# Optimization experiments

Measured on AMD Instinct MI355X. Metric: run time of the kernel, lower is better.

The kernel has to match this reference:

```python
import jax, jax.numpy as jnp
import numpy as np

B, NORB, N_UP, N_DN, HIDDEN = 1024, 128, 32, 32, 4096


def setup_inputs() -> dict:
    rng = np.random.default_rng(0)
    # Build valid occupancy configs: exactly N_UP up-electrons (bit 0) and
    # N_DN down-electrons (bit 1) per sample. Encoding: 0=empty,1=up,2=dn,3=updn.
    up_order = np.argsort(rng.random((B, NORB)), axis=1)
    dn_order = np.argsort(rng.random((B, NORB)), axis=1)
    up_bit = np.zeros((B, NORB), np.int32)
    dn_bit = np.zeros((B, NORB), np.int32)
    np.put_along_axis(up_bit, up_order[:, :N_UP], 1, axis=1)
    np.put_along_axis(dn_bit, dn_order[:, :N_DN], 1, axis=1)
    x = jnp.asarray(up_bit + 2 * dn_bit, dtype=jnp.int32)

    key = jax.random.key(0)
    k1, k2, k3 = jax.random.split(key, 3)
    orbitals = jax.random.normal(k1, (NORB, N_UP), jnp.float32)
    W1 = jax.random.normal(k2, (4 * NORB, HIDDEN), jnp.float32) / np.sqrt(4 * NORB)
    b1 = jnp.zeros((HIDDEN,), jnp.float32)
    W2 = jax.random.normal(k3, (HIDDEN, NORB * N_UP), jnp.float32) / np.sqrt(HIDDEN)
    b2 = jnp.zeros((NORB * N_UP,), jnp.float32)
    return {"x": x, "orbitals": orbitals, "W1": W1, "b1": b1, "W2": W2, "b2": b2}


def _occupancies_to_electrons(x, n_up, n_dn):
    # Per-spin sorted positions of occupied orbitals. Stable argsort on the
    # inverted mask keeps occupied sites first, in ascending orbital order.
    up_mask = (x & 1) == 1
    dn_mask = (x & 2) == 2
    y_up = jnp.argsort(jnp.where(up_mask, 0, 1), axis=-1, stable=True)[:, :n_up]
    y_dn = jnp.argsort(jnp.where(dn_mask, 0, 1), axis=-1, stable=True)[:, :n_dn]
    return y_up, y_dn


def reference(x, orbitals, W1, b1, W2, b2):
    Bsz, norb = x.shape
    n_up = orbitals.shape[1]

    # correction_fun: MLP on one-hot config -> [B, norb, n_up]
    h = jax.nn.one_hot(x, 4, dtype=W1.dtype).reshape(Bsz, -1)  # [B, 4*norb]
    h = jax.nn.relu(h @ W1 + b1)                               # [B, hidden]
    corrections = (h @ W2 + b2).reshape(Bsz, norb, n_up)       # [B, norb, n_up]

    y_up, y_dn = _occupancies_to_electrons(x, n_up, n_up)
    y_up = y_up[..., None]  # [B, n_up, 1]
    y_dn = y_dn[..., None]

    # gather orbital rows + correction rows per electron (spin-symmetric orbitals)
    phi_up = jnp.take_along_axis(orbitals[None], y_up, axis=1)  # [B, n_up, n_up]
    phi_dn = jnp.take_along_axis(orbitals[None], y_dn, axis=1)
    d_up = jnp.take_along_axis(corrections, y_up, axis=1)
    d_dn = jnp.take_along_axis(corrections, y_dn, axis=1)

    s_up, log_det_up = jnp.linalg.slogdet(phi_up + d_up)
    s_dn, log_det_dn = jnp.linalg.slogdet(phi_dn + d_dn)
    return log_det_up + log_det_dn + jnp.log(s_up * s_dn + 0j)  # complex [B]
```

## Files before the change

kernel.cpp:

```cpp
#include <hip/hip_runtime.h>
#include <cmath>

#define B_SZ  1024
#define NORB  128
#define NUP   32
#define HID   4096
#define NCORR (NORB * NUP)
#define K1    (4 * NORB)

typedef short  bf16x8 __attribute__((ext_vector_type(8)));
typedef float  f32x4  __attribute__((ext_vector_type(4)));

__device__ __forceinline__ unsigned short f2bf_rne(float f) {
    unsigned int u = __float_as_uint(f);
    u += 0x7FFFu + ((u >> 16) & 1u);
    return (unsigned short)(u >> 16);
}

__global__ __launch_bounds__(256) void k_splitW(const float* __restrict__ W,
                                                unsigned short* __restrict__ Bph,
                                                unsigned short* __restrict__ Bpl,
                                                int ktTot) {
    __shared__ float tile[64][33];
    int n0 = blockIdx.x * 32, k0 = blockIdx.y * 64;
    int t = threadIdx.x;

    int rl = t >> 3, c4 = (t & 7) * 4;
#pragma unroll
    for (int i = 0; i < 2; ++i) {
        int kl = rl + 32 * i;
        float4 v = *(const float4*)(W + (size_t)(k0 + kl) * 4096 + n0 + c4);
        tile[kl][c4 + 0] = v.x; tile[kl][c4 + 1] = v.y;
        tile[kl][c4 + 2] = v.z; tile[kl][c4 + 3] = v.w;
    }
    __syncthreads();

    int nl = t & 31, kg = t >> 5;
    int nt = (n0 + nl) >> 4;
    int kt = (k0 >> 5) + (kg >> 2);
    int lane_o = (kg & 3) * 16 + (nl & 15);
    size_t o = (((size_t)nt * ktTot + kt) * 64 + lane_o) * 8;

    unsigned short hi8[8], lo8[8];
#pragma unroll
    for (int j = 0; j < 8; ++j) {
        float v = tile[kg * 8 + j][nl];
        unsigned short hi = f2bf_rne(v);
        float fhi = __uint_as_float((unsigned int)hi << 16);
        hi8[j] = hi;
        lo8[j] = f2bf_rne(v - fhi);
    }
    *(bf16x8*)(Bph + o) = *(bf16x8*)hi8;
    *(bf16x8*)(Bpl + o) = *(bf16x8*)lo8;
}

__global__ __launch_bounds__(256, 2) void k_hidden3(const int* __restrict__ x,
                                                    const unsigned short* __restrict__ Bph,
                                                    const unsigned short* __restrict__ Bpl,
                                                    const float* __restrict__ b1,
                                                    unsigned short* __restrict__ h_hi,
                                                    unsigned short* __restrict__ h_lo) {
    __shared__ unsigned int sxp[64][8];
    __shared__ unsigned short BF[2][4][4][512];
    __shared__ float Ht[64][132];

    int n0 = blockIdx.x * 128;
    int m0 = blockIdx.y * 64;
    int t = threadIdx.x;
    int w = t >> 6, lane = t & 63;
    int lm = lane & 15, kq = lane >> 4;
    int wn = w * 32;

#pragma unroll
    for (int i = 0; i < 2; ++i) {
        int id = t + 256 * i;
        int row = id >> 3, d = id & 7;
        const int* src = x + (size_t)(m0 + row) * NORB + d * 16;
        unsigned int dw = 0;
#pragma unroll
        for (int b = 0; b < 16; ++b) dw |= ((unsigned int)(src[b] & 3)) << (2 * b);
        sxp[row][d] = dw;
    }

    int nt0 = (n0 + wn) >> 4;
    const unsigned short* bh0 = Bph + (size_t)nt0 * (16 * 512) + (size_t)lane * 8;
    const unsigned short* bh1 = Bph + (size_t)(nt0 + 1) * (16 * 512) + (size_t)lane * 8;
    const unsigned short* bl0 = Bpl + (size_t)nt0 * (16 * 512) + (size_t)lane * 8;
    const unsigned short* bl1 = Bpl + (size_t)(nt0 + 1) * (16 * 512) + (size_t)lane * 8;

    f32x4 acc[4][2] = {};

    bf16x8 r0 = *(const bf16x8*)(bh0);
    bf16x8 r1 = *(const bf16x8*)(bh1);
    bf16x8 r2 = *(const bf16x8*)(bl0);
    bf16x8 r3 = *(const bf16x8*)(bl1);
    bf16x8 r4 = *(const bf16x8*)(bh0 + 512);
    bf16x8 r5 = *(const bf16x8*)(bh1 + 512);
    bf16x8 r6 = *(const bf16x8*)(bl0 + 512);
    bf16x8 r7 = *(const bf16x8*)(bl1 + 512);

    __syncthreads();

    for (int p = 0; p < 8; ++p) {
        if (p) __syncthreads();

        *(bf16x8*)&BF[0][w][0][lane * 8] = r0;
        *(bf16x8*)&BF[0][w][1][lane * 8] = r1;
        *(bf16x8*)&BF[0][w][2][lane * 8] = r2;
        *(bf16x8*)&BF[0][w][3][lane * 8] = r3;
        *(bf16x8*)&BF[1][w][0][lane * 8] = r4;
        *(bf16x8*)&BF[1][w][1][lane * 8] = r5;
        *(bf16x8*)&BF[1][w][2][lane * 8] = r6;
        *(bf16x8*)&BF[1][w][3][lane * 8] = r7;
        __syncthreads();

        int kn = (p + 1 < 8) ? p + 1 : 7;
        r0 = *(const bf16x8*)(bh0 + (2 * kn) * 512);
        r1 = *(const bf16x8*)(bh1 + (2 * kn) * 512);
        r2 = *(const bf16x8*)(bl0 + (2 * kn) * 512);
        r3 = *(const bf16x8*)(bl1 + (2 * kn) * 512);
        r4 = *(const bf16x8*)(bh0 + (2 * kn + 1) * 512);
        r5 = *(const bf16x8*)(bh1 + (2 * kn + 1) * 512);
        r6 = *(const bf16x8*)(bl0 + (2 * kn + 1) * 512);
        r7 = *(const bf16x8*)(bl1 + (2 * kn + 1) * 512);

#pragma unroll
        for (int s = 0; s < 2; ++s) {
            int kt = 2 * p + s;
            int i0 = kt * 8 + kq * 2;
            int dwIdx = i0 >> 4;
            int sh = (i0 & 15) * 2;
            bf16x8 af[4];
#pragma unroll
            for (int fm = 0; fm < 4; ++fm) {
                unsigned int dw = sxp[fm * 16 + lm][dwIdx];
                unsigned int c01 = (dw >> sh) & 0xFu;
                union { bf16x8 v; unsigned long long u[2]; } a;
                a.u[0] = 0x3F80ULL << ((c01 & 3u) * 16);
                a.u[1] = 0x3F80ULL << ((c01 >> 2) * 16);
                af[fm] = a.v;
            }

            bf16x8 b0h = *(const bf16x8*)&BF[s][w][0][lane * 8];
            bf16x8 b1h = *(const bf16x8*)&BF[s][w][1][lane * 8];
            bf16x8 b0l = *(const bf16x8*)&BF[s][w][2][lane * 8];
            bf16x8 b1l = *(const bf16x8*)&BF[s][w][3][lane * 8];

#pragma unroll
            for (int fm = 0; fm < 4; ++fm) {
                acc[fm][0] = __builtin_amdgcn_mfma_f32_16x16x32_bf16(af[fm], b0h, acc[fm][0], 0, 0, 0);
                acc[fm][0] = __builtin_amdgcn_mfma_f32_16x16x32_bf16(af[fm], b0l, acc[fm][0], 0, 0, 0);
                acc[fm][1] = __builtin_amdgcn_mfma_f32_16x16x32_bf16(af[fm], b1h, acc[fm][1], 0, 0, 0);
                acc[fm][1] = __builtin_amdgcn_mfma_f32_16x16x32_bf16(af[fm], b1l, acc[fm][1], 0, 0, 0);
            }
        }
    }

    __syncthreads();
#pragma unroll
    for (int fm = 0; fm < 4; ++fm)
#pragma unroll
        for (int fn = 0; fn < 2; ++fn) {
            int n = wn + fn * 16 + lm;
            float bv = b1[n0 + n];
#pragma unroll
            for (int r = 0; r < 4; ++r)
                Ht[fm * 16 + kq * 4 + r][n] = fmaxf(acc[fm][fn][r] + bv, 0.f);
        }
    __syncthreads();

    size_t mt0 = (size_t)(m0 >> 4), kt0 = (size_t)(n0 >> 5);
#pragma unroll
    for (int fi = 0; fi < 4; ++fi) {
        int f = w * 4 + fi;
        int mt = f >> 2, ktn = f & 3;
        int m = mt * 16 + lm;
        int kn = ktn * 32 + kq * 8;
        float4 v0 = *(const float4*)&Ht[m][kn];
        float4 v1 = *(const float4*)&Ht[m][kn + 4];
        float vv[8] = {v0.x, v0.y, v0.z, v0.w, v1.x, v1.y, v1.z, v1.w};
        unsigned short hi8[8], lo8[8];
#pragma unroll
        for (int j = 0; j < 8; ++j) {
            unsigned short hi = f2bf_rne(vv[j]);
            float fhi = __uint_as_float((unsigned int)hi << 16);
            hi8[j] = hi;
            lo8[j] = f2bf_rne(vv[j] - fhi);
        }
        size_t o = (((mt0 + mt) * 128 + (kt0 + ktn)) * 64 + lane) * 8;
        *(bf16x8*)(h_hi + o) = *(bf16x8*)hi8;
        *(bf16x8*)(h_lo + o) = *(bf16x8*)lo8;
    }
}

__global__ __launch_bounds__(256) void k_hidden_f32(const int* __restrict__ x,
                                                    const float* __restrict__ W1,
                                                    const float* __restrict__ b1,
                                                    float* __restrict__ h) {
    int b = blockIdx.x, tid = threadIdx.x;
    __shared__ int sx[NORB];
    if (tid < NORB) sx[tid] = x[b * NORB + tid];
    __syncthreads();
    float acc[16];
#pragma unroll
    for (int u = 0; u < 16; ++u) acc[u] = b1[tid + 256 * u];
    for (int i = 0; i < NORB; ++i) {
        const float* row = W1 + (size_t)(4 * i + sx[i]) * HID;
#pragma unroll
        for (int u = 0; u < 16; ++u) acc[u] += row[tid + 256 * u];
    }
    float* hb = h + (size_t)b * HID;
#pragma unroll
    for (int u = 0; u < 16; ++u) hb[tid + 256 * u] = fmaxf(acc[u], 0.f);
}

__global__ __launch_bounds__(256, 2) void k_gemm6(const unsigned short* __restrict__ Ahp,
                                                  const unsigned short* __restrict__ Alp,
                                                  const unsigned short* __restrict__ Bph,
                                                  const unsigned short* __restrict__ Bpl,
                                                  const float* __restrict__ bias,
                                                  float* __restrict__ C) {
    __shared__ unsigned short AF[2][2][4][512];

    int n0 = blockIdx.x * 128;
    int m0 = blockIdx.y * 64;
    int t = threadIdx.x;
    int w = t >> 6, lane = t & 63;
    int lm = lane & 15, kq = lane >> 4;
    int wn = w * 32;

    int mt0 = m0 >> 4;
    int nt0 = (n0 + wn) >> 4;

    const unsigned short* agh = Ahp + (size_t)(mt0 + w) * 65536 + (size_t)lane * 8;
    const unsigned short* agl = Alp + (size_t)(mt0 + w) * 65536 + (size_t)lane * 8;
    const unsigned short* bh0 = Bph + (size_t)nt0 * 65536 + (size_t)lane * 8;
    const unsigned short* bh1 = Bph + (size_t)(nt0 + 1) * 65536 + (size_t)lane * 8;
    const unsigned short* bl0 = Bpl + (size_t)nt0 * 65536 + (size_t)lane * 8;
    const unsigned short* bl1 = Bpl + (size_t)(nt0 + 1) * 65536 + (size_t)lane * 8;

    f32x4 acc[4][2] = {};

    float4 rh0 = *(const float4*)(agh);
    float4 rh1 = *(const float4*)(agh + 512);
    float4 rl0 = *(const float4*)(agl);
    float4 rl1 = *(const float4*)(agl + 512);

    for (int ktp = 0; ktp < 64; ++ktp) {
        if (ktp) __syncthreads();

        int o0 = (2 * ktp) * 512, o1 = o0 + 512;
        bf16x8 B00h = *(const bf16x8*)(bh0 + o0);
        bf16x8 B01h = *(const bf16x8*)(bh1 + o0);
        bf16x8 B00l = *(const bf16x8*)(bl0 + o0);
        bf16x8 B01l = *(const bf16x8*)(bl1 + o0);
        bf16x8 B10h = *(const bf16x8*)(bh0 + o1);
        bf16x8 B11h = *(const bf16x8*)(bh1 + o1);
        bf16x8 B10l = *(const bf16x8*)(bl0 + o1);
        bf16x8 B11l = *(const bf16x8*)(bl1 + o1);

        *(float4*)&AF[0][0][w][lane * 8] = rh0;
        *(float4*)&AF[1][0][w][lane * 8] = rh1;
        *(float4*)&AF[0][1][w][lane * 8] = rl0;
        *(float4*)&AF[1][1][w][lane * 8] = rl1;
        __syncthreads();

        int kn = (ktp + 1 < 64) ? ktp + 1 : 63;
        rh0 = *(const float4*)(agh + (size_t)(2 * kn) * 512);
        rh1 = *(const float4*)(agh + (size_t)(2 * kn + 1) * 512);
        rl0 = *(const float4*)(agl + (size_t)(2 * kn) * 512);
        rl1 = *(const float4*)(agl + (size_t)(2 * kn + 1) * 512);

        bf16x8 ah[4], al[4];
#pragma unroll
        for (int fm = 0; fm < 4; ++fm) {
            ah[fm] = *(const bf16x8*)&AF[0][0][fm][lane * 8];
            al[fm] = *(const bf16x8*)&AF[0][1][fm][lane * 8];
        }
#pragma unroll
        for (int fm = 0; fm < 4; ++fm) {
            acc[fm][0] = __builtin_amdgcn_mfma_f32_16x16x32_bf16(ah[fm], B00h, acc[fm][0], 0, 0, 0);
            acc[fm][0] = __builtin_amdgcn_mfma_f32_16x16x32_bf16(al[fm], B00h, acc[fm][0], 0, 0, 0);
            acc[fm][0] = __builtin_amdgcn_mfma_f32_16x16x32_bf16(ah[fm], B00l, acc[fm][0], 0, 0, 0);
            acc[fm][1] = __builtin_amdgcn_mfma_f32_16x16x32_bf16(ah[fm], B01h, acc[fm][1], 0, 0, 0);
            acc[fm][1] = __builtin_amdgcn_mfma_f32_16x16x32_bf16(al[fm], B01h, acc[fm][1], 0, 0, 0);
            acc[fm][1] = __builtin_amdgcn_mfma_f32_16x16x32_bf16(ah[fm], B01l, acc[fm][1], 0, 0, 0);
        }

#pragma unroll
        for (int fm = 0; fm < 4; ++fm) {
            ah[fm] = *(const bf16x8*)&AF[1][0][fm][lane * 8];
            al[fm] = *(const bf16x8*)&AF[1][1][fm][lane * 8];
        }
#pragma unroll
        for (int fm = 0; fm < 4; ++fm) {
            acc[fm][0] = __builtin_amdgcn_mfma_f32_16x16x32_bf16(ah[fm], B10h, acc[fm][0], 0, 0, 0);
            acc[fm][0] = __builtin_amdgcn_mfma_f32_16x16x32_bf16(al[fm], B10h, acc[fm][0], 0, 0, 0);
            acc[fm][0] = __builtin_amdgcn_mfma_f32_16x16x32_bf16(ah[fm], B10l, acc[fm][0], 0, 0, 0);
            acc[fm][1] = __builtin_amdgcn_mfma_f32_16x16x32_bf16(ah[fm], B11h, acc[fm][1], 0, 0, 0);
            acc[fm][1] = __builtin_amdgcn_mfma_f32_16x16x32_bf16(al[fm], B11h, acc[fm][1], 0, 0, 0);
            acc[fm][1] = __builtin_amdgcn_mfma_f32_16x16x32_bf16(ah[fm], B11l, acc[fm][1], 0, 0, 0);
        }
    }

#pragma unroll
    for (int fm = 0; fm < 4; ++fm)
#pragma unroll
        for (int fn = 0; fn < 2; ++fn) {
            int n = n0 + wn + fn * 16 + lm;
            float bv = bias[n];
#pragma unroll
            for (int r = 0; r < 4; ++r) {
                int m = m0 + fm * 16 + kq * 4 + r;
                C[(size_t)m * NCORR + n] = acc[fm][fn][r] + bv;
            }
        }
}

#define BM 64
#define BN 64
#define BK 32
__global__ __launch_bounds__(256) void k_gemm(const float* __restrict__ A,
                                              const float* __restrict__ Bm,
                                              const float* __restrict__ bias,
                                              float* __restrict__ C) {
    __shared__ float As[BK][68];
    __shared__ float Bs[BK][BN];
    int n0 = blockIdx.x * BN, m0 = blockIdx.y * BM;
    int tid = threadIdx.x;
    int tm = tid >> 4, tn = tid & 15;
    int am = tid >> 3, ak = (tid & 7) * 4;
    int bk = tid >> 4, bn = (tid & 15) * 4;
    float acc[4][4] = {};
    for (int k0 = 0; k0 < HID; k0 += BK) {
#pragma unroll
        for (int s = 0; s < 2; ++s) {
            int m = am + 32 * s;
            float4 v = *(const float4*)(A + (size_t)(m0 + m) * HID + k0 + ak);
            As[ak + 0][m] = v.x; As[ak + 1][m] = v.y;
            As[ak + 2][m] = v.z; As[ak + 3][m] = v.w;
        }
#pragma unroll
        for (int s = 0; s < 2; ++s) {
            int k = bk + 16 * s;
            float4 v = *(const float4*)(Bm + (size_t)(k0 + k) * NCORR + n0 + bn);
            *(float4*)&Bs[k][bn] = v;
        }
        __syncthreads();
#pragma unroll
        for (int kk = 0; kk < BK; ++kk) {
            float4 a = *(const float4*)&As[kk][tm * 4];
            float4 bv = *(const float4*)&Bs[kk][tn * 4];
            float av[4] = {a.x, a.y, a.z, a.w};
            float bb[4] = {bv.x, bv.y, bv.z, bv.w};
#pragma unroll
            for (int i = 0; i < 4; ++i)
#pragma unroll
                for (int j = 0; j < 4; ++j) acc[i][j] += av[i] * bb[j];
        }
        __syncthreads();
    }
#pragma unroll
    for (int i = 0; i < 4; ++i) {
        int m = m0 + tm * 4 + i;
        float4 o;
        o.x = acc[i][0] + bias[n0 + tn * 4 + 0];
        o.y = acc[i][1] + bias[n0 + tn * 4 + 1];
        o.z = acc[i][2] + bias[n0 + tn * 4 + 2];
        o.w = acc[i][3] + bias[n0 + tn * 4 + 3];
        *(float4*)(C + (size_t)m * NCORR + n0 + tn * 4) = o;
    }
}

__global__ __launch_bounds__(128) void k_det(const int* __restrict__ x,
                                             const float* __restrict__ orbitals,
                                             const float* __restrict__ corr,
                                             float* __restrict__ out,
                                             int imag_off) {
    int b = blockIdx.x, tid = threadIdx.x;
    __shared__ int sx[NORB];
    __shared__ int yup[NUP], ydn[NUP];
    __shared__ float M[2][NUP][NUP + 1];
    __shared__ float rlog[2];
    __shared__ int rneg[2];

    sx[tid] = x[b * NORB + tid];
    __syncthreads();

    int occ = sx[tid];
    if (occ & 1) {
        int r = 0;
        for (int i = 0; i < tid; ++i) r += sx[i] & 1;
        yup[r] = tid;
    }
    if (occ & 2) {
        int r = 0;
        for (int i = 0; i < tid; ++i) r += (sx[i] >> 1) & 1;
        ydn[r] = tid;
    }
    __syncthreads();

    const float* cb = corr + (size_t)b * NCORR;
    for (int idx = tid; idx < 2 * NUP * NUP; idx += 128) {
        int s = idx >> 10;
        int i = (idx >> 5) & 31;
        int j = idx & 31;
        int r = s ? ydn[i] : yup[i];
        M[s][i][j] = orbitals[r * NUP + j] + cb[r * NUP + j];
    }
    __syncthreads();

    int wv = tid >> 6, lane = tid & 63;
    float (*Mm)[NUP + 1] = M[wv];
    float logdet = 0.f;
    int neg = 0;

    for (int k = 0; k < NUP; ++k) {
        float v = (lane >= k && lane < NUP) ? fabsf(Mm[lane][k]) : -1.f;
        int pi = lane;
#pragma unroll
        for (int off = 32; off > 0; off >>= 1) {
            float v2 = __shfl_down(v, off);
            int p2 = __shfl_down(pi, off);
            if (v2 > v) { v = v2; pi = p2; }
        }
        int p = __shfl(pi, 0);

        if (p != k) {
            if (lane < NUP) {
                float t1 = Mm[k][lane];
                Mm[k][lane] = Mm[p][lane];
                Mm[p][lane] = t1;
            }
            neg ^= 1;
        }
        __syncthreads();

        float pv = Mm[k][k];
        logdet += logf(fabsf(pv));
        if (pv < 0.f) neg ^= 1;

        int row = k + 1 + (lane & 31);
        int half = lane >> 5;
        if (row < NUP) {
            float f = Mm[row][k] / pv;
            for (int j = k + 1 + half; j < NUP; j += 2)
                Mm[row][j] -= f * Mm[k][j];
        }
        __syncthreads();
    }

    if (lane == 0) { rlog[wv] = logdet; rneg[wv] = neg; }
    __syncthreads();
    if (tid == 0) {
        out[b] = rlog[0] + rlog[1];
        if (imag_off > 0)
            out[imag_off + b] =
                (rneg[0] ^ rneg[1]) ? 3.14159265358979323846f : 0.f;
    }
}

extern "C" void kernel_launch(void* const* d_in, const int* in_sizes, int n_in,
                              void* d_out, int out_size, void* d_ws, size_t ws_size,
                              hipStream_t stream) {
    const int*   x        = (const int*)d_in[0];
    const float* orbitals = (const float*)d_in[1];
    const float* W1       = (const float*)d_in[2];
    const float* b1       = (const float*)d_in[3];
    const float* W2       = (const float*)d_in[4];
    const float* b2       = (const float*)d_in[5];
    float* out = (float*)d_out;
    int imag_off = (out_size == 2 * B_SZ) ? B_SZ : 0;

    const size_t need = (size_t)96 * 1024 * 1024;
    if (ws_size >= need) {
        unsigned short* h_hi = (unsigned short*)d_ws;
        unsigned short* h_lo = h_hi + (size_t)B_SZ * HID;
        unsigned short* Bph  = h_lo + (size_t)B_SZ * HID;
        unsigned short* Bpl  = Bph + (size_t)HID * NCORR;
        float*          corr = (float*)(Bpl + (size_t)HID * NCORR);

        unsigned short* W1ph = (unsigned short*)corr;
        unsigned short* W1pl = W1ph + (size_t)K1 * HID;

        k_splitW<<<dim3(HID / 32, K1 / 64), 256, 0, stream>>>(W1, W1ph, W1pl, 16);
        k_splitW<<<dim3(NCORR / 32, HID / 64), 256, 0, stream>>>(W2, Bph, Bpl, 128);

        k_hidden3<<<dim3(HID / 128, B_SZ / 64), 256, 0, stream>>>(x, W1ph, W1pl, b1, h_hi, h_lo);

        dim3 g2(NCORR / 128, B_SZ / 64);
        k_gemm6<<<g2, 256, 0, stream>>>(h_hi, h_lo, Bph, Bpl, b2, corr);
        k_det<<<B_SZ, 128, 0, stream>>>(x, orbitals, corr, out, imag_off);
    } else {
        float* h    = (float*)d_ws;
        float* corr = h + (size_t)B_SZ * HID;
        k_hidden_f32<<<B_SZ, 256, 0, stream>>>(x, W1, b1, h);
        dim3 g2(NCORR / BN, B_SZ / BM);
        k_gemm<<<g2, 256, 0, stream>>>(h, W2, b2, corr);
        k_det<<<B_SZ, 128, 0, stream>>>(x, orbitals, corr, out, imag_off);
    }
}
```

Measured before the change: 264.8 us.

## Switch second GEMM to fp16 split with scaled low part and single-fp16 activations

Replaces the three-pass bf16 hi/lo split GEMM with fp16 MFMAs. The activations are stored as a single fp16 array, and W2 is split into an fp16 high part plus a low residual scaled by 2048, so each tile needs two MFMAs instead of three and half the A traffic. The low part goes into a separate accumulator and is rescaled in the epilogue. This drops the activation residual term, which risks precision loss if hidden values exceed fp16 range or need more mantissa than fp16 offers.

```diff
diff --git a/kernel.cpp b/kernel.cpp
--- a/kernel.cpp
+++ b/kernel.cpp
@@ -8,8 +8,9 @@
 #define NCORR (NORB * NUP)
 #define K1    (4 * NORB)
 
-typedef short  bf16x8 __attribute__((ext_vector_type(8)));
-typedef float  f32x4  __attribute__((ext_vector_type(4)));
+typedef short    bf16x8 __attribute__((ext_vector_type(8)));
+typedef _Float16 f16x8  __attribute__((ext_vector_type(8)));
+typedef float    f32x4  __attribute__((ext_vector_type(4)));
 
 __device__ __forceinline__ unsigned short f2bf_rne(float f) {
     unsigned int u = __float_as_uint(f);
@@ -54,12 +55,46 @@
     *(bf16x8*)(Bpl + o) = *(bf16x8*)lo8;
 }
 
+__global__ __launch_bounds__(256) void k_splitW16(const float* __restrict__ W,
+                                                  _Float16* __restrict__ Bph,
+                                                  _Float16* __restrict__ Bpl) {
+    __shared__ float tile[64][33];
+    int n0 = blockIdx.x * 32, k0 = blockIdx.y * 64;
+    int t = threadIdx.x;
+
+    int rl = t >> 3, c4 = (t & 7) * 4;
+#pragma unroll
+    for (int i = 0; i < 2; ++i) {
+        int kl = rl + 32 * i;
+        float4 v = *(const float4*)(W + (size_t)(k0 + kl) * 4096 + n0 + c4);
+        tile[kl][c4 + 0] = v.x; tile[kl][c4 + 1] = v.y;
+        tile[kl][c4 + 2] = v.z; tile[kl][c4 + 3] = v.w;
+    }
+    __syncthreads();
+
+    int nl = t & 31, kg = t >> 5;
+    int nt = (n0 + nl) >> 4;
+    int kt = (k0 >> 5) + (kg >> 2);
+    int lane_o = (kg & 3) * 16 + (nl & 15);
+    size_t o = (((size_t)nt * 128 + kt) * 64 + lane_o) * 8;
+
+    f16x8 hi8, lo8;
+#pragma unroll
+    for (int j = 0; j < 8; ++j) {
+        float v = tile[kg * 8 + j][nl];
+        _Float16 hi = (_Float16)v;
+        hi8[j] = hi;
+        lo8[j] = (_Float16)((v - (float)hi) * 2048.0f);
+    }
+    *(f16x8*)(Bph + o) = hi8;
+    *(f16x8*)(Bpl + o) = lo8;
+}
+
 __global__ __launch_bounds__(256, 2) void k_hidden3(const int* __restrict__ x,
                                                     const unsigned short* __restrict__ Bph,
                                                     const unsigned short* __restrict__ Bpl,
                                                     const float* __restrict__ b1,
-                                                    unsigned short* __restrict__ h_hi,
-                                                    unsigned short* __restrict__ h_lo) {
+                                                    _Float16* __restrict__ h16) {
     __shared__ unsigned int sxp[64][8];
     __shared__ unsigned short BF[2][4][4][512];
     __shared__ float Ht[64][132];
@@ -179,17 +214,11 @@
         float4 v0 = *(const float4*)&Ht[m][kn];
         float4 v1 = *(const float4*)&Ht[m][kn + 4];
         float vv[8] = {v0.x, v0.y, v0.z, v0.w, v1.x, v1.y, v1.z, v1.w};
-        unsigned short hi8[8], lo8[8];
-#pragma unroll
-        for (int j = 0; j < 8; ++j) {
-            unsigned short hi = f2bf_rne(vv[j]);
-            float fhi = __uint_as_float((unsigned int)hi << 16);
-            hi8[j] = hi;
-            lo8[j] = f2bf_rne(vv[j] - fhi);
-        }
+        f16x8 o16;
+#pragma unroll
+        for (int j = 0; j < 8; ++j) o16[j] = (_Float16)vv[j];
         size_t o = (((mt0 + mt) * 128 + (kt0 + ktn)) * 64 + lane) * 8;
-        *(bf16x8*)(h_hi + o) = *(bf16x8*)hi8;
-        *(bf16x8*)(h_lo + o) = *(bf16x8*)lo8;
+        *(f16x8*)(h16 + o) = o16;
     }
 }
 
@@ -214,13 +243,12 @@
     for (int u = 0; u < 16; ++u) hb[tid + 256 * u] = fmaxf(acc[u], 0.f);
 }
 
-__global__ __launch_bounds__(256, 2) void k_gemm6(const unsigned short* __restrict__ Ahp,
-                                                  const unsigned short* __restrict__ Alp,
-                                                  const unsigned short* __restrict__ Bph,
-                                                  const unsigned short* __restrict__ Bpl,
+__global__ __launch_bounds__(256, 2) void k_gemm7(const _Float16* __restrict__ Ap,
+                                                  const _Float16* __restrict__ Bph,
+                                                  const _Float16* __restrict__ Bpl,
                                                   const float* __restrict__ bias,
                                                   float* __restrict__ C) {
-    __shared__ unsigned short AF[2][2][4][512];
+    __shared__ _Float16 AF[2][4][512];
 
     int n0 = blockIdx.x * 128;
     int m0 = blockIdx.y * 64;
@@ -232,77 +260,62 @@
     int mt0 = m0 >> 4;
     int nt0 = (n0 + wn) >> 4;
 
-    const unsigned short* agh = Ahp + (size_t)(mt0 + w) * 65536 + (size_t)lane * 8;
-    const unsigned short* agl = Alp + (size_t)(mt0 + w) * 65536 + (size_t)lane * 8;
-    const unsigned short* bh0 = Bph + (size_t)nt0 * 65536 + (size_t)lane * 8;
-    const unsigned short* bh1 = Bph + (size_t)(nt0 + 1) * 65536 + (size_t)lane * 8;
-    const unsigned short* bl0 = Bpl + (size_t)nt0 * 65536 + (size_t)lane * 8;
-    const unsigned short* bl1 = Bpl + (size_t)(nt0 + 1) * 65536 + (size_t)lane * 8;
-
-    f32x4 acc[4][2] = {};
-
-    float4 rh0 = *(const float4*)(agh);
-    float4 rh1 = *(const float4*)(agh + 512);
-    float4 rl0 = *(const float4*)(agl);
-    float4 rl1 = *(const float4*)(agl + 512);
+    const _Float16* ag  = Ap  + (size_t)(mt0 + w) * 65536 + (size_t)lane * 8;
+    const _Float16* bh0 = Bph + (size_t)nt0 * 65536 + (size_t)lane * 8;
+    const _Float16* bh1 = Bph + (size_t)(nt0 + 1) * 65536 + (size_t)lane * 8;
+    const _Float16* bl0 = Bpl + (size_t)nt0 * 65536 + (size_t)lane * 8;
+    const _Float16* bl1 = Bpl + (size_t)(nt0 + 1) * 65536 + (size_t)lane * 8;
+
+    f32x4 accH[4][2] = {}, accL[4][2] = {};
+
+    f16x8 r0 = *(const f16x8*)(ag);
+    f16x8 r1 = *(const f16x8*)(ag + 512);
 
     for (int ktp = 0; ktp < 64; ++ktp) {
         if (ktp) __syncthreads();
 
         int o0 = (2 * ktp) * 512, o1 = o0 + 512;
-        bf16x8 B00h = *(const bf16x8*)(bh0 + o0);
-        bf16x8 B01h = *(const bf16x8*)(bh1 + o0);
-        bf16x8 B00l = *(const bf16x8*)(bl0 + o0);
-        bf16x8 B01l = *(const bf16x8*)(bl1 + o0);
-        bf16x8 B10h = *(const bf16x8*)(bh0 + o1);
-        bf16x8 B11h = *(const bf16x8*)(bh1 + o1);
-        bf16x8 B10l = *(const bf16x8*)(bl0 + o1);
-        bf16x8 B11l = *(const bf16x8*)(bl1 + o1);
-
-        *(float4*)&AF[0][0][w][lane * 8] = rh0;
-        *(float4*)&AF[1][0][w][lane * 8] = rh1;
-        *(float4*)&AF[0][1][w][lane * 8] = rl0;
-        *(float4*)&AF[1][1][w][lane * 8] = rl1;
+        f16x8 B0h0 = *(const f16x8*)(bh0 + o0);
+        f16x8 B0h1 = *(const f16x8*)(bh1 + o0);
+        f16x8 B0l0 = *(const f16x8*)(bl0 + o0);
+        f16x8 B0l1 = *(const f16x8*)(bl1 + o0);
+        f16x8 B1h0 = *(const f16x8*)(bh0 + o1);
+        f16x8 B1h1 = *(const f16x8*)(bh1 + o1);
+        f16x8 B1l0 = *(const f16x8*)(bl0 + o1);
+        f16x8 B1l1 = *(const f16x8*)(bl1 + o1);
+
+        *(f16x8*)&AF[0][w][lane * 8] = r0;
+        *(f16x8*)&AF[1][w][lane * 8] = r1;
         __syncthreads();
 
         int kn = (ktp + 1 < 64) ? ktp + 1 : 63;
-        rh0 = *(const float4*)(agh + (size_t)(2 * kn) * 512);
-        rh1 = *(const float4*)(agh + (size_t)(2 * kn + 1) * 512);
-        rl0 = *(const float4*)(agl + (size_t)(2 * kn) * 512);
-        rl1 = *(const float4*)(agl + (size_t)(2 * kn + 1) * 512);
-
-        bf16x8 ah[4], al[4];
+        r0 = *(const f16x8*)(ag + (size_t)(2 * kn) * 512);
+        r1 = *(const f16x8*)(ag + (size_t)(2 * kn + 1) * 512);
+
+        f16x8 a0[4], a1[4];
 #pragma unroll
         for (int fm = 0; fm < 4; ++fm) {
-            ah[fm] = *(const bf16x8*)&AF[0][0][fm][lane * 8];
-            al[fm] = *(const bf16x8*)&AF[0][1][fm][lane * 8];
-        }
+            a0[fm] = *(const f16x8*)&AF[0][fm][lane * 8];
+            a1[fm] = *(const f16x8*)&AF[1][fm][lane * 8];
+        }
+
 #pragma unroll
         for (int fm = 0; fm < 4; ++fm) {
-            acc[fm][0] = __builtin_amdgcn_mfma_f32_16x16x32_bf16(ah[fm], B00h, acc[fm][0], 0, 0, 0);
-            acc[fm][0] = __builtin_amdgcn_mfma_f32_16x16x32_bf16(al[fm], B00h, acc[fm][0], 0, 0, 0);
-            acc[fm][0] = __builtin_amdgcn_mfma_f32_16x16x32_bf16(ah[fm], B00l, acc[fm][0], 0, 0, 0);
-            acc[fm][1] = __builtin_amdgcn_mfma_f32_16x16x32_bf16(ah[fm], B01h, acc[fm][1], 0, 0, 0);
-            acc[fm][1] = __builtin_amdgcn_mfma_f32_16x16x32_bf16(al[fm], B01h, acc[fm][1], 0, 0, 0);
-            acc[fm][1] = __builtin_amdgcn_mfma_f32_16x16x32_bf16(ah[fm], B01l, acc[fm][1], 0, 0, 0);
-        }
-
+            accH[fm][0] = __builtin_amdgcn_mfma_f32_16x16x32_f16(a0[fm], B0h0, accH[fm][0], 0, 0, 0);
+            accL[fm][0] = __builtin_amdgcn_mfma_f32_16x16x32_f16(a0[fm], B0l0, accL[fm][0], 0, 0, 0);
+            accH[fm][1] = __builtin_amdgcn_mfma_f32_16x16x32_f16(a0[fm], B0h1, accH[fm][1], 0, 0, 0);
+            accL[fm][1] = __builtin_amdgcn_mfma_f32_16x16x32_f16(a0[fm], B0l1, accL[fm][1], 0, 0, 0);
+        }
 #pragma unroll
         for (int fm = 0; fm < 4; ++fm) {
-            ah[fm] = *(const bf16x8*)&AF[1][0][fm][lane * 8];
-            al[fm] = *(const bf16x8*)&AF[1][1][fm][lane * 8];
-        }
-#pragma unroll
-        for (int fm = 0; fm < 4; ++fm) {
-            acc[fm][0] = __builtin_amdgcn_mfma_f32_16x16x32_bf16(ah[fm], B10h, acc[fm][0], 0, 0, 0);
-            acc[fm][0] = __builtin_amdgcn_mfma_f32_16x16x32_bf16(al[fm], B10h, acc[fm][0], 0, 0, 0);
-            acc[fm][0] = __builtin_amdgcn_mfma_f32_16x16x32_bf16(ah[fm], B10l, acc[fm][0], 0, 0, 0);
-            acc[fm][1] = __builtin_amdgcn_mfma_f32_16x16x32_bf16(ah[fm], B11h, acc[fm][1], 0, 0, 0);
-            acc[fm][1] = __builtin_amdgcn_mfma_f32_16x16x32_bf16(al[fm], B11h, acc[fm][1], 0, 0, 0);
-            acc[fm][1] = __builtin_amdgcn_mfma_f32_16x16x32_bf16(ah[fm], B11l, acc[fm][1], 0, 0, 0);
-        }
-    }
-
+            accH[fm][0] = __builtin_amdgcn_mfma_f32_16x16x32_f16(a1[fm], B1h0, accH[fm][0], 0, 0, 0);
+            accL[fm][0] = __builtin_amdgcn_mfma_f32_16x16x32_f16(a1[fm], B1l0, accL[fm][0], 0, 0, 0);
+            accH[fm][1] = __builtin_amdgcn_mfma_f32_16x16x32_f16(a1[fm], B1h1, accH[fm][1], 0, 0, 0);
+            accL[fm][1] = __builtin_amdgcn_mfma_f32_16x16x32_f16(a1[fm], B1l1, accL[fm][1], 0, 0, 0);
+        }
+    }
+
+    const float ls = 1.0f / 2048.0f;
 #pragma unroll
     for (int fm = 0; fm < 4; ++fm)
 #pragma unroll
@@ -312,7 +325,7 @@
 #pragma unroll
             for (int r = 0; r < 4; ++r) {
                 int m = m0 + fm * 16 + kq * 4 + r;
-                C[(size_t)m * NCORR + n] = acc[fm][fn][r] + bv;
+                C[(size_t)m * NCORR + n] = accH[fm][fn][r] + ls * accL[fm][fn][r] + bv;
             }
         }
 }
@@ -474,22 +487,21 @@
 
     const size_t need = (size_t)96 * 1024 * 1024;
     if (ws_size >= need) {
-        unsigned short* h_hi = (unsigned short*)d_ws;
-        unsigned short* h_lo = h_hi + (size_t)B_SZ * HID;
-        unsigned short* Bph  = h_lo + (size_t)B_SZ * HID;
-        unsigned short* Bpl  = Bph + (size_t)HID * NCORR;
-        float*          corr = (float*)(Bpl + (size_t)HID * NCORR);
+        _Float16* h16  = (_Float16*)d_ws;
+        _Float16* Bh16 = h16 + (size_t)B_SZ * HID;
+        _Float16* Bl16 = Bh16 + (size_t)HID * NCORR;
+        float*    corr = (float*)(Bl16 + (size_t)HID * NCORR);
 
         unsigned short* W1ph = (unsigned short*)corr;
         unsigned short* W1pl = W1ph + (size_t)K1 * HID;
 
         k_splitW<<<dim3(HID / 32, K1 / 64), 256, 0, stream>>>(W1, W1ph, W1pl, 16);
-        k_splitW<<<dim3(NCORR / 32, HID / 64), 256, 0, stream>>>(W2, Bph, Bpl, 128);
-
-        k_hidden3<<<dim3(HID / 128, B_SZ / 64), 256, 0, stream>>>(x, W1ph, W1pl, b1, h_hi, h_lo);
+        k_splitW16<<<dim3(NCORR / 32, HID / 64), 256, 0, stream>>>(W2, Bh16, Bl16);
+
+        k_hidden3<<<dim3(HID / 128, B_SZ / 64), 256, 0, stream>>>(x, W1ph, W1pl, b1, h16);
 
         dim3 g2(NCORR / 128, B_SZ / 64);
-        k_gemm6<<<g2, 256, 0, stream>>>(h_hi, h_lo, Bph, Bpl, b2, corr);
+        k_gemm7<<<g2, 256, 0, stream>>>(h16, Bh16, Bl16, b2, corr);
         k_det<<<B_SZ, 128, 0, stream>>>(x, orbitals, corr, out, imag_off);
     } else {
         float* h    = (float*)d_ws;
```

Result: faster. 239.5 us (-9.6%).
